# Optimization experiments

Hardware: AMD Instinct MI355X
Metric: run time of the kernel (lower is better)

## Reference

```python
import jax, jax.numpy as jnp
import numpy as np

NUM_USERS = 100000
NUM_ITEMS = 50000
EMB_DIM = 64
NNZ = 4800000
BATCH = 16384
N_LAYERS = 3


def setup_inputs() -> dict:
    key = jax.random.key(0)
    k0, k1, k2, k3, k4, k5 = jax.random.split(key, 6)
    N = NUM_USERS + NUM_ITEMS
    rows = jax.random.randint(k0, (NNZ,), 0, N, dtype=jnp.int32)
    cols = jax.random.randint(k1, (NNZ,), 0, N, dtype=jnp.int32)
    # symmetric normalization values: 1/sqrt(deg_out * deg_in), as in LightGCN preprocessing
    ones = jnp.ones((NNZ,), jnp.float32)
    deg_r = jax.ops.segment_sum(ones, rows, num_segments=N)
    deg_c = jax.ops.segment_sum(ones, cols, num_segments=N)
    vals = 1.0 / jnp.sqrt(jnp.maximum(deg_r[rows], 1.0) * jnp.maximum(deg_c[cols], 1.0))
    user_emb = 0.1 * jax.random.normal(k2, (NUM_USERS, EMB_DIM), jnp.float32)
    item_emb = 0.1 * jax.random.normal(k3, (NUM_ITEMS, EMB_DIM), jnp.float32)
    user_idx = jax.random.randint(k4, (BATCH,), 0, NUM_USERS, dtype=jnp.int64)
    item_idx = jax.random.randint(k5, (BATCH,), 0, NUM_ITEMS, dtype=jnp.int64)
    return {
        "user_emb": user_emb,
        "item_emb": item_emb,
        "rows": rows,
        "cols": cols,
        "vals": vals,
        "user_idx": user_idx,
        "item_idx": item_idx,
        "n_layers": N_LAYERS,
    }


def reference(user_emb, item_emb, rows, cols, vals, user_idx, item_idx, n_layers):
    num_users = user_emb.shape[0]
    N = num_users + item_emb.shape[0]
    all_emb = jnp.concatenate([user_emb, item_emb], axis=0)  # [N, D]
    acc = all_emb  # running sum over layer embeddings (embs[0] = E)
    emb = all_emb
    for _ in range(n_layers):
        # SpMM: out[r] = sum_{edges (r,c)} vals * emb[c]
        emb = jax.ops.segment_sum(vals[:, None] * emb[cols], rows, num_segments=N)
        acc = acc + emb
    light_out = acc / jnp.float32(n_layers + 1)  # mean over stacked layers
    u_e = light_out[user_idx]                     # [B, D]
    i_e = light_out[num_users + item_idx]         # [B, D]
    return (u_e * i_e).sum(axis=-1)               # [B]
```

## Files before the change

### kernel.cpp

```cpp
#include <hip/hip_runtime.h>
#include <hip/hip_fp16.h>

#define NUM_USERS 100000
#define NUM_ITEMS 50000
#define NN (NUM_USERS + NUM_ITEMS)
#define EMB_DIM 64
#define BATCH 16384
#define RPA 512
#define NBA ((NN + RPA - 1) / RPA)
#define SLOT 22528
#define NBLKA 768
#define CAP 16
#define OVF 32
#define SENT (1 << 27)
#define RSLOT 72
#define RPB 256
#define LSLOT 64
#define NBB (NBA * 2)

__device__ __forceinline__ unsigned h2u(__half2 h) {
    union { __half2 h; unsigned u; } x; x.h = h; return x.u;
}
__device__ __forceinline__ __half2 u2h(unsigned u) {
    union { __half2 h; unsigned u; } x; x.u = u; return x.h;
}

__global__ void lgcn_prep(unsigned long long* __restrict__ gq,
                          unsigned char* __restrict__ flags) {
    int i = blockIdx.x * blockDim.x + threadIdx.x;
    if (i < NBA) gq[i] = 0;
    for (int j = i; j < NN / 4; j += gridDim.x * blockDim.x)
        ((unsigned*)flags)[j] = 0;
    if (i == 0)
        for (int j = (NN / 4) * 4; j < NN; ++j) flags[j] = 0;
}

__global__ void __launch_bounds__(512) lgcn_binA(
        const float4* __restrict__ user_emb, const float4* __restrict__ item_emb,
        uint2* __restrict__ embh, int n_user4, int n_tot4,
        const int* __restrict__ rows, const int* __restrict__ cols,
        const float* __restrict__ vals, unsigned long long* __restrict__ gq,
        int2* __restrict__ cv_tmp, int nnz, int epb) {
    __shared__ int2 stage[CAP][NBA];
    __shared__ int  hist[NBA];
    __shared__ int  SBase[NBA];
    __shared__ int  pcnt[NBA];
    __shared__ int4 ovfBuf[2][OVF];
    __shared__ int  ovfCnt[2];
    int t = threadIdx.x;

    for (int i = blockIdx.x * 512 + t; i < n_tot4; i += NBLKA * 512) {
        float4 v = (i < n_user4) ? user_emb[i] : item_emb[i - n_user4];
        uint2 o;
        o.x = h2u(__float22half2_rn(make_float2(v.x, v.y)));
        o.y = h2u(__float22half2_rn(make_float2(v.z, v.w)));
        embh[i] = o;
    }

    int base = blockIdx.x * epb;
    int end  = base + epb; if (end > nnz) end = nnz;
    if (t < NBA) { hist[t] = 0; pcnt[t] = 0; }
    if (t == 0) { ovfCnt[0] = 0; ovfCnt[1] = 0; }
    __syncthreads();
    for (int i = base + t; i < end; i += 512)
        atomicAdd(&hist[rows[i] >> 9], 1);
    __syncthreads();
    if (t < NBA) {
        int c = hist[t];
        int p = 0;
        if (c) {
            int cp = (c + 7) & ~7;
            unsigned long long old = atomicAdd(&gq[t],
                ((unsigned long long)c << 32) | (unsigned)cp);
            p = (int)(unsigned)old;
        }
        SBase[t] = p;
    }
    __syncthreads();

    int p = 0;
    for (int r0 = base; r0 < end; r0 += 1024, p ^= 1) {
        int no = ovfCnt[p ^ 1];
        for (int j = t; j < no; j += 512) {
            int4 e = ovfBuf[p ^ 1][j];
            int b = e.w;
            int k = atomicAdd(&pcnt[b], 1);
            if (k < CAP) stage[k][b] = make_int2(e.x, e.y);
            else { int q = atomicAdd(&ovfCnt[p], 1);
                   if (q < OVF) ovfBuf[p][q] = e; }
        }
#pragma unroll
        for (int q2 = 0; q2 < 2; ++q2) {
            int i = r0 + q2 * 512 + t;
            if (i < end) {
                int r = rows[i];
                int b = r >> 9;
                __half hv = __float2half(vals[i]);
                int ex = ((r & 511) << 18) | cols[i];
                int ey = (int)h2u(__half2half2(hv));
                int k = atomicAdd(&pcnt[b], 1);
                if (k < CAP) stage[k][b] = make_int2(ex, ey);
                else { int q = atomicAdd(&ovfCnt[p], 1);
                       if (q < OVF) ovfBuf[p][q] = make_int4(ex, ey, 0, b); }
            }
        }
        __syncthreads();
        if (t < NBA) {
            int c = pcnt[t]; if (c > CAP) c = CAP;
            int g = c & ~7;
            if (g) {
                long long gb = (long long)t * SLOT + SBase[t];
                int4* dst = (int4*)&cv_tmp[gb];
                for (int j = 0; j < g; j += 2) {
                    int2 e0 = stage[j][t];
                    int2 e1 = stage[j + 1][t];
                    dst[j >> 1] = make_int4(e0.x, e0.y, e1.x, e1.y);
                }
                SBase[t] += g;
                for (int j = g; j < c; ++j) stage[j - g][t] = stage[j][t];
            }
            pcnt[t] = c - g;
        }
        if (t == 0) ovfCnt[p ^ 1] = 0;
        __syncthreads();
    }

    {
        int no = ovfCnt[p ^ 1];
        for (int j = t; j < no; j += 512) {
            int4 e = ovfBuf[p ^ 1][j];
            int b = e.w;
            int k = atomicAdd(&pcnt[b], 1);
            if (k < CAP) stage[k][b] = make_int2(e.x, e.y);
            else cv_tmp[(long long)b * SLOT + SBase[b] + k] =
                     make_int2(e.x, e.y);
        }
    }
    __syncthreads();
    if (t < NBA) {
        int c_raw = pcnt[t];
        int cl = min(c_raw, CAP);
        long long gb = (long long)t * SLOT + SBase[t];
        for (int j = 0; j < cl; ++j) cv_tmp[gb + j] = stage[j][t];
        int cp = (c_raw + 7) & ~7;
        for (int j = c_raw; j < cp; ++j) cv_tmp[gb + j] = make_int2(SENT, 0);
    }
}

#define BPUT(p) do { int x = (p).x; if (!(x & SENT)) {                       \
    int rl9 = (x >> 18) & 511;                                               \
    if ((rl9 & 256) == hsel) { int rl = rl9 & 255;                           \
        int pos = atomicAdd(&cnt[rl], 1);                                    \
        int v16 = (p).y & 0xFFFF;                                            \
        int pk = (((v16 + 2) >> 2) << 18) | (x & 0x3FFFF);                   \
        if (pos < LSLOT) slot[rl][pos] = pk;                                 \
        else if (pos < RSLOT)                                                \
            cv[(long long)(r0 + rl) * RSLOT + pos] = pk; } } } while (0)

__global__ void __launch_bounds__(1024) lgcn_binB(
        const unsigned long long* __restrict__ gq,
        const int2* __restrict__ cv_tmp, int* __restrict__ cv,
        int* __restrict__ deg,
        const int* __restrict__ user_idx, const int* __restrict__ item_idx,
        unsigned char* __restrict__ flags) {
    __shared__ int slot[RPB][LSLOT];
    __shared__ int cnt[RPB];
    int s    = blockIdx.x >> 1;
    int half = blockIdx.x & 1;
    int t = threadIdx.x;
    long long w0 = (long long)s * SLOT;
    int wlen = (int)(unsigned)gq[s];
    int r0 = s * RPA + half * RPB;
    int hsel = half << 8;
    for (int j = t; j < RPB; j += 1024) cnt[j] = 0;
    __syncthreads();
    int i = t;
    for (; i + 3 * 1024 < wlen; i += 4096) {
        int2 p0 = cv_tmp[w0 + i];
        int2 p1 = cv_tmp[w0 + i + 1024];
        int2 p2 = cv_tmp[w0 + i + 2048];
        int2 p3 = cv_tmp[w0 + i + 3072];
        BPUT(p0); BPUT(p1); BPUT(p2); BPUT(p3);
    }
    for (; i < wlen; i += 1024) {
        int2 p = cv_tmp[w0 + i];
        BPUT(p);
    }
    for (int j = blockIdx.x * 1024 + t; j < BATCH; j += NBB * 1024) {
        flags[user_idx[j]] = 1;
        flags[NUM_USERS + item_idx[j]] = 1;
    }
    __syncthreads();
    for (int j = t; j < RPB; j += 1024) deg[r0 + j] = min(cnt[j], RSLOT);
    for (int g = t; g < RPB * (LSLOT / 4); g += 1024) {
        int rl = g >> 4, q = g & 15;
        int4 v = *(int4*)&slot[rl][q * 4];
        *(int4*)&cv[(long long)(r0 + rl) * RSLOT + q * 4] = v;
    }
}

__device__ __forceinline__ unsigned eidx(int p, int dim8) {
    return ((unsigned)p & 0x3FFFFu) * 8u + (unsigned)dim8;
}
__device__ __forceinline__ void efma(int p, uint4 raw,
        __half2& c0, __half2& c1, __half2& c2, __half2& c3) {
    unsigned vv = ((unsigned)p >> 18) << 2;
    __half2 v2 = u2h(vv | (vv << 16));
    c0 = __hfma2(v2, u2h(raw.x), c0);
    c1 = __hfma2(v2, u2h(raw.y), c1);
    c2 = __hfma2(v2, u2h(raw.z), c2);
    c3 = __hfma2(v2, u2h(raw.w), c3);
}

__global__ void __launch_bounds__(256) lgcn_spmm(
        const int* __restrict__ deg,
        const int* __restrict__ cv,
        const uint4* __restrict__ embh,
        uint4* __restrict__ nxth,
        const unsigned char* __restrict__ flags, int sel,
        const uint4* __restrict__ e0t, const uint4* __restrict__ e1t,
        float4* __restrict__ sums) {
    int wid = (blockIdx.x * blockDim.x + threadIdx.x) >> 6;
    int lane = threadIdx.x & 63;
    if (wid >= NN) return;
    if (sel && !flags[wid]) return;
    int n = deg[wid];
    int grp  = lane >> 3;
    int dim8 = lane & 7;
    const int* ep = cv + wid * RSLOT;

    __half2 c0 = __float2half2_rn(0.f);
    __half2 c1 = c0, c2 = c0, c3 = c0;

    int nb = n >> 5;
    if (nb == 2) {
        int4 pa = *(const int4*)&ep[4 * grp];
        int4 pb = *(const int4*)&ep[32 + 4 * grp];
        uint4 ra0 = embh[eidx(pa.x, dim8)];
        uint4 ra1 = embh[eidx(pa.y, dim8)];
        uint4 ra2 = embh[eidx(pa.z, dim8)];
        uint4 ra3 = embh[eidx(pa.w, dim8)];
        uint4 rb0 = embh[eidx(pb.x, dim8)];
        uint4 rb1 = embh[eidx(pb.y, dim8)];
        uint4 rb2 = embh[eidx(pb.z, dim8)];
        uint4 rb3 = embh[eidx(pb.w, dim8)];
        efma(pa.x, ra0, c0, c1, c2, c3);
        efma(pa.y, ra1, c0, c1, c2, c3);
        efma(pa.z, ra2, c0, c1, c2, c3);
        efma(pa.w, ra3, c0, c1, c2, c3);
        efma(pb.x, rb0, c0, c1, c2, c3);
        efma(pb.y, rb1, c0, c1, c2, c3);
        efma(pb.z, rb2, c0, c1, c2, c3);
        efma(pb.w, rb3, c0, c1, c2, c3);
    } else if (nb == 1) {
        int4 pa = *(const int4*)&ep[4 * grp];
        uint4 ra0 = embh[eidx(pa.x, dim8)];
        uint4 ra1 = embh[eidx(pa.y, dim8)];
        uint4 ra2 = embh[eidx(pa.z, dim8)];
        uint4 ra3 = embh[eidx(pa.w, dim8)];
        efma(pa.x, ra0, c0, c1, c2, c3);
        efma(pa.y, ra1, c0, c1, c2, c3);
        efma(pa.z, ra2, c0, c1, c2, c3);
        efma(pa.w, ra3, c0, c1, c2, c3);
    }
    const int* et = ep + (nb << 5);
    int rem = n & 31;
    if (rem & 16) {
        int2 p2 = *(const int2*)&et[2 * grp];
        uint4 ra = embh[eidx(p2.x, dim8)];
        uint4 rb = embh[eidx(p2.y, dim8)];
        efma(p2.x, ra, c0, c1, c2, c3);
        efma(p2.y, rb, c0, c1, c2, c3);
        et += 16;
    }
    if (rem & 8) {
        int pp = et[grp];
        uint4 rr = embh[eidx(pp, dim8)];
        efma(pp, rr, c0, c1, c2, c3);
        et += 8;
    }
    int r7 = rem & 7;
    if (grp < r7) {
        int pp = et[grp];
        uint4 rr = embh[eidx(pp, dim8)];
        efma(pp, rr, c0, c1, c2, c3);
    }

#pragma unroll
    for (int off = 8; off < 64; off <<= 1) {
        c0 = __hadd2(c0, u2h(__shfl_xor(h2u(c0), off)));
        c1 = __hadd2(c1, u2h(__shfl_xor(h2u(c1), off)));
        c2 = __hadd2(c2, u2h(__shfl_xor(h2u(c2), off)));
        c3 = __hadd2(c3, u2h(__shfl_xor(h2u(c3), off)));
    }
    if (grp == 0) {
        int o = wid * 8 + dim8;
        if (!sel) {
            uint4 ov;
            ov.x = h2u(c0); ov.y = h2u(c1); ov.z = h2u(c2); ov.w = h2u(c3);
            nxth[o] = ov;
        } else {
            uint4 r0v = e0t[o], r1v = e1t[o], r2v = embh[o];
            float2 f0 = __half22float2(c0), f1 = __half22float2(c1);
            float2 f2 = __half22float2(c2), f3 = __half22float2(c3);
            float2 a;
            a = __half22float2(u2h(r0v.x)); f0.x += a.x; f0.y += a.y;
            a = __half22float2(u2h(r1v.x)); f0.x += a.x; f0.y += a.y;
            a = __half22float2(u2h(r2v.x)); f0.x += a.x; f0.y += a.y;
            a = __half22float2(u2h(r0v.y)); f1.x += a.x; f1.y += a.y;
            a = __half22float2(u2h(r1v.y)); f1.x += a.x; f1.y += a.y;
            a = __half22float2(u2h(r2v.y)); f1.x += a.x; f1.y += a.y;
            a = __half22float2(u2h(r0v.z)); f2.x += a.x; f2.y += a.y;
            a = __half22float2(u2h(r1v.z)); f2.x += a.x; f2.y += a.y;
            a = __half22float2(u2h(r2v.z)); f2.x += a.x; f2.y += a.y;
            a = __half22float2(u2h(r0v.w)); f3.x += a.x; f3.y += a.y;
            a = __half22float2(u2h(r1v.w)); f3.x += a.x; f3.y += a.y;
            a = __half22float2(u2h(r2v.w)); f3.x += a.x; f3.y += a.y;
            int so = wid * 16 + dim8 * 2;
            sums[so]     = make_float4(f0.x, f0.y, f1.x, f1.y);
            sums[so + 1] = make_float4(f2.x, f2.y, f3.x, f3.y);
        }
    }
}

__global__ void lgcn_dot(const float4* __restrict__ sums,
                         const int* __restrict__ user_idx,
                         const int* __restrict__ item_idx,
                         float* __restrict__ out, int batch) {
    int t = blockIdx.x * blockDim.x + threadIdx.x;
    int b = t >> 4;
    if (b >= batch) return;
    int l = t & 15;
    float4 su = sums[(long long)user_idx[b] * 16 + l];
    float4 si = sums[(long long)(NUM_USERS + item_idx[b]) * 16 + l];
    float s = su.x * si.x + su.y * si.y + su.z * si.z + su.w * si.w;
    s += __shfl_down(s, 8, 16);
    s += __shfl_down(s, 4, 16);
    s += __shfl_down(s, 2, 16);
    s += __shfl_down(s, 1, 16);
    if (l == 0) out[b] = s * (1.0f / 16.0f);
}

extern "C" void kernel_launch(void* const* d_in, const int* in_sizes, int n_in,
                              void* d_out, int out_size, void* d_ws, size_t ws_size,
                              hipStream_t stream) {
    const float* user_emb = (const float*)d_in[0];
    const float* item_emb = (const float*)d_in[1];
    const int*   rows     = (const int*)d_in[2];
    const int*   cols     = (const int*)d_in[3];
    const float* vals     = (const float*)d_in[4];
    const int*   user_idx = (const int*)d_in[5];
    const int*   item_idx = (const int*)d_in[6];
    float* out = (float*)d_out;

    const int nnz = in_sizes[2];
    const size_t node_uint2 = (size_t)NN * 16;

    uint2* E[4];
    E[0] = (uint2*)d_ws;
    E[1] = E[0] + node_uint2;
    E[2] = E[1] + node_uint2;
    E[3] = E[2] + node_uint2;
    int*    cv   = (int*)(E[3] + node_uint2);
    float4* sums = (float4*)(cv + (size_t)NN * RSLOT);
    int*    deg  = (int*)(sums + (size_t)NN * 16);
    unsigned long long* gq = (unsigned long long*)(deg + NN);
    unsigned char* flags = (unsigned char*)(gq + NBA);
    int2*   cv_tmp = (int2*)E[1];

    const int n_tot4  = NN * EMB_DIM / 4;
    const int n_user4 = NUM_USERS * EMB_DIM / 4;
    const int epb = (nnz + NBLKA - 1) / NBLKA;

    lgcn_prep<<<64, 256, 0, stream>>>(gq, flags);

    lgcn_binA<<<NBLKA, 512, 0, stream>>>(
        (const float4*)user_emb, (const float4*)item_emb, E[0],
        n_user4, n_tot4, rows, cols, vals, gq, cv_tmp, nnz, epb);

    lgcn_binB<<<NBB, 1024, 0, stream>>>(gq, cv_tmp, cv, deg,
                                        user_idx, item_idx, flags);

    const int spmm_blocks = (NN * 64 + 255) / 256;
    for (int layer = 0; layer < 3; ++layer) {
        lgcn_spmm<<<spmm_blocks, 256, 0, stream>>>(deg, cv,
                                                   (const uint4*)E[layer],
                                                   (uint4*)E[layer + 1],
                                                   flags, layer == 2 ? 1 : 0,
                                                   (const uint4*)E[0],
                                                   (const uint4*)E[1], sums);
    }

    lgcn_dot<<<(BATCH * 16 + 255) / 256, 256, 0, stream>>>(
        sums, user_idx, item_idx, out, BATCH);
}
```

Baseline: 390.9 us.

## Fuse first SpMM into binning kernel and last layer into batch dot

Layer-1 SpMM now runs inside the binB kernel, reading each row's edge list straight from shared memory right after binning, which removes one full SpMM launch and a pass over the cv array. The final layer is computed only for batch rows inside a new dot kernel that also sums the layer embeddings, which removes the flags array, its clearing, the sums buffer and the separate dot kernel. The catch is that binB runs a serial per-warp row loop without unrolled gathers. Batch rows are also recomputed whenever an index repeats.

```diff
diff --git a/kernel.cpp b/kernel.cpp
--- a/kernel.cpp
+++ b/kernel.cpp
@@ -24,15 +24,22 @@
 __device__ __forceinline__ __half2 u2h(unsigned u) {
     union { __half2 h; unsigned u; } x; x.u = u; return x.h;
 }
-
-__global__ void lgcn_prep(unsigned long long* __restrict__ gq,
-                          unsigned char* __restrict__ flags) {
+__device__ __forceinline__ unsigned eidx(int p, int dim8) {
+    return ((unsigned)p & 0x3FFFFu) * 8u + (unsigned)dim8;
+}
+__device__ __forceinline__ void efma(int p, uint4 raw,
+        __half2& c0, __half2& c1, __half2& c2, __half2& c3) {
+    unsigned vv = ((unsigned)p >> 18) << 2;
+    __half2 v2 = u2h(vv | (vv << 16));
+    c0 = __hfma2(v2, u2h(raw.x), c0);
+    c1 = __hfma2(v2, u2h(raw.y), c1);
+    c2 = __hfma2(v2, u2h(raw.z), c2);
+    c3 = __hfma2(v2, u2h(raw.w), c3);
+}
+
+__global__ void lgcn_prep(unsigned long long* __restrict__ gq) {
     int i = blockIdx.x * blockDim.x + threadIdx.x;
     if (i < NBA) gq[i] = 0;
-    for (int j = i; j < NN / 4; j += gridDim.x * blockDim.x)
-        ((unsigned*)flags)[j] = 0;
-    if (i == 0)
-        for (int j = (NN / 4) * 4; j < NN; ++j) flags[j] = 0;
 }
 
 __global__ void __launch_bounds__(512) lgcn_binA(
@@ -155,14 +162,14 @@
         int pk = (((v16 + 2) >> 2) << 18) | (x & 0x3FFFF);                   \
         if (pos < LSLOT) slot[rl][pos] = pk;                                 \
         else if (pos < RSLOT)                                                \
-            cv[(long long)(r0 + rl) * RSLOT + pos] = pk; } } } while (0)
-
-__global__ void __launch_bounds__(1024) lgcn_binB(
+            cv[(r0 + rl) * RSLOT + pos] = pk; } } } while (0)
+
+__global__ void __launch_bounds__(1024) lgcn_binBspmm1(
         const unsigned long long* __restrict__ gq,
         const int2* __restrict__ cv_tmp, int* __restrict__ cv,
         int* __restrict__ deg,
-        const int* __restrict__ user_idx, const int* __restrict__ item_idx,
-        unsigned char* __restrict__ flags) {
+        const uint4* __restrict__ embh,
+        uint4* __restrict__ outB) {
     __shared__ int slot[RPB][LSLOT];
     __shared__ int cnt[RPB];
     int s    = blockIdx.x >> 1;
@@ -186,44 +193,60 @@
         int2 p = cv_tmp[w0 + i];
         BPUT(p);
     }
-    for (int j = blockIdx.x * 1024 + t; j < BATCH; j += NBB * 1024) {
-        flags[user_idx[j]] = 1;
-        flags[NUM_USERS + item_idx[j]] = 1;
-    }
-    __syncthreads();
-    for (int j = t; j < RPB; j += 1024) deg[r0 + j] = min(cnt[j], RSLOT);
+    __syncthreads();
+    for (int j = t; j < RPB; j += 1024)
+        if (r0 + j < NN) deg[r0 + j] = min(cnt[j], RSLOT);
     for (int g = t; g < RPB * (LSLOT / 4); g += 1024) {
         int rl = g >> 4, q = g & 15;
-        int4 v = *(int4*)&slot[rl][q * 4];
-        *(int4*)&cv[(long long)(r0 + rl) * RSLOT + q * 4] = v;
-    }
-}
-
-__device__ __forceinline__ unsigned eidx(int p, int dim8) {
-    return ((unsigned)p & 0x3FFFFu) * 8u + (unsigned)dim8;
-}
-__device__ __forceinline__ void efma(int p, uint4 raw,
-        __half2& c0, __half2& c1, __half2& c2, __half2& c3) {
-    unsigned vv = ((unsigned)p >> 18) << 2;
-    __half2 v2 = u2h(vv | (vv << 16));
-    c0 = __hfma2(v2, u2h(raw.x), c0);
-    c1 = __hfma2(v2, u2h(raw.y), c1);
-    c2 = __hfma2(v2, u2h(raw.z), c2);
-    c3 = __hfma2(v2, u2h(raw.w), c3);
+        if (r0 + rl < NN) {
+            int4 v = *(int4*)&slot[rl][q * 4];
+            *(int4*)&cv[(r0 + rl) * RSLOT + q * 4] = v;
+        }
+    }
+    int w = t >> 6, lane = t & 63;
+    int grp = lane >> 3, dim8 = lane & 7;
+    for (int rr = w * 16; rr < w * 16 + 16; ++rr) {
+        int r = r0 + rr;
+        if (r >= NN) continue;
+        int n = min(cnt[rr], RSLOT);
+        __half2 c0 = __float2half2_rn(0.f);
+        __half2 c1 = c0, c2 = c0, c3 = c0;
+        int m = n >> 3;
+        for (int k = 0; k < m; ++k) {
+            int j = 8 * k + grp;
+            int p = (j < LSLOT) ? slot[rr][j] : cv[r * RSLOT + j];
+            uint4 raw = embh[eidx(p, dim8)];
+            efma(p, raw, c0, c1, c2, c3);
+        }
+        if (grp < (n & 7)) {
+            int j = 8 * m + grp;
+            int p = (j < LSLOT) ? slot[rr][j] : cv[r * RSLOT + j];
+            uint4 raw = embh[eidx(p, dim8)];
+            efma(p, raw, c0, c1, c2, c3);
+        }
+#pragma unroll
+        for (int off = 8; off < 64; off <<= 1) {
+            c0 = __hadd2(c0, u2h(__shfl_xor(h2u(c0), off)));
+            c1 = __hadd2(c1, u2h(__shfl_xor(h2u(c1), off)));
+            c2 = __hadd2(c2, u2h(__shfl_xor(h2u(c2), off)));
+            c3 = __hadd2(c3, u2h(__shfl_xor(h2u(c3), off)));
+        }
+        if (grp == 0) {
+            uint4 ov;
+            ov.x = h2u(c0); ov.y = h2u(c1); ov.z = h2u(c2); ov.w = h2u(c3);
+            outB[r * 8 + dim8] = ov;
+        }
+    }
 }
 
 __global__ void __launch_bounds__(256) lgcn_spmm(
         const int* __restrict__ deg,
         const int* __restrict__ cv,
         const uint4* __restrict__ embh,
-        uint4* __restrict__ nxth,
-        const unsigned char* __restrict__ flags, int sel,
-        const uint4* __restrict__ e0t, const uint4* __restrict__ e1t,
-        float4* __restrict__ sums) {
+        uint4* __restrict__ nxth) {
     int wid = (blockIdx.x * blockDim.x + threadIdx.x) >> 6;
     int lane = threadIdx.x & 63;
     if (wid >= NN) return;
-    if (sel && !flags[wid]) return;
     int n = deg[wid];
     int grp  = lane >> 3;
     int dim8 = lane & 7;
@@ -294,51 +317,79 @@
         c3 = __hadd2(c3, u2h(__shfl_xor(h2u(c3), off)));
     }
     if (grp == 0) {
-        int o = wid * 8 + dim8;
-        if (!sel) {
-            uint4 ov;
-            ov.x = h2u(c0); ov.y = h2u(c1); ov.z = h2u(c2); ov.w = h2u(c3);
-            nxth[o] = ov;
-        } else {
-            uint4 r0v = e0t[o], r1v = e1t[o], r2v = embh[o];
-            float2 f0 = __half22float2(c0), f1 = __half22float2(c1);
-            float2 f2 = __half22float2(c2), f3 = __half22float2(c3);
-            float2 a;
-            a = __half22float2(u2h(r0v.x)); f0.x += a.x; f0.y += a.y;
-            a = __half22float2(u2h(r1v.x)); f0.x += a.x; f0.y += a.y;
-            a = __half22float2(u2h(r2v.x)); f0.x += a.x; f0.y += a.y;
-            a = __half22float2(u2h(r0v.y)); f1.x += a.x; f1.y += a.y;
-            a = __half22float2(u2h(r1v.y)); f1.x += a.x; f1.y += a.y;
-            a = __half22float2(u2h(r2v.y)); f1.x += a.x; f1.y += a.y;
-            a = __half22float2(u2h(r0v.z)); f2.x += a.x; f2.y += a.y;
-            a = __half22float2(u2h(r1v.z)); f2.x += a.x; f2.y += a.y;
-            a = __half22float2(u2h(r2v.z)); f2.x += a.x; f2.y += a.y;
-            a = __half22float2(u2h(r0v.w)); f3.x += a.x; f3.y += a.y;
-            a = __half22float2(u2h(r1v.w)); f3.x += a.x; f3.y += a.y;
-            a = __half22float2(u2h(r2v.w)); f3.x += a.x; f3.y += a.y;
-            int so = wid * 16 + dim8 * 2;
-            sums[so]     = make_float4(f0.x, f0.y, f1.x, f1.y);
-            sums[so + 1] = make_float4(f2.x, f2.y, f3.x, f3.y);
-        }
-    }
-}
-
-__global__ void lgcn_dot(const float4* __restrict__ sums,
-                         const int* __restrict__ user_idx,
-                         const int* __restrict__ item_idx,
-                         float* __restrict__ out, int batch) {
-    int t = blockIdx.x * blockDim.x + threadIdx.x;
-    int b = t >> 4;
-    if (b >= batch) return;
-    int l = t & 15;
-    float4 su = sums[(long long)user_idx[b] * 16 + l];
-    float4 si = sums[(long long)(NUM_USERS + item_idx[b]) * 16 + l];
-    float s = su.x * si.x + su.y * si.y + su.z * si.z + su.w * si.w;
-    s += __shfl_down(s, 8, 16);
-    s += __shfl_down(s, 4, 16);
-    s += __shfl_down(s, 2, 16);
-    s += __shfl_down(s, 1, 16);
-    if (l == 0) out[b] = s * (1.0f / 16.0f);
+        uint4 ov;
+        ov.x = h2u(c0); ov.y = h2u(c1); ov.z = h2u(c2); ov.w = h2u(c3);
+        nxth[wid * 8 + dim8] = ov;
+    }
+}
+
+__device__ __forceinline__ void d3row(const int* __restrict__ cv,
+        const int* __restrict__ deg, const uint4* __restrict__ C,
+        const uint4* __restrict__ A, const uint4* __restrict__ B,
+        int r, int grp, int dim8,
+        float2& f0, float2& f1, float2& f2, float2& f3) {
+    int n = deg[r];
+    const int* ep = cv + r * RSLOT;
+    __half2 c0 = __float2half2_rn(0.f);
+    __half2 c1 = c0, c2 = c0, c3 = c0;
+    int m = n >> 3;
+    for (int k = 0; k < m; ++k) {
+        int p = ep[8 * k + grp];
+        uint4 raw = C[eidx(p, dim8)];
+        efma(p, raw, c0, c1, c2, c3);
+    }
+    if (grp < (n & 7)) {
+        int p = ep[8 * m + grp];
+        uint4 raw = C[eidx(p, dim8)];
+        efma(p, raw, c0, c1, c2, c3);
+    }
+#pragma unroll
+    for (int off = 8; off < 64; off <<= 1) {
+        c0 = __hadd2(c0, u2h(__shfl_xor(h2u(c0), off)));
+        c1 = __hadd2(c1, u2h(__shfl_xor(h2u(c1), off)));
+        c2 = __hadd2(c2, u2h(__shfl_xor(h2u(c2), off)));
+        c3 = __hadd2(c3, u2h(__shfl_xor(h2u(c3), off)));
+    }
+    f0 = __half22float2(c0); f1 = __half22float2(c1);
+    f2 = __half22float2(c2); f3 = __half22float2(c3);
+    int o = r * 8 + dim8;
+    uint4 ra = A[o], rb = B[o], rc = C[o];
+    float2 a;
+    a = __half22float2(u2h(ra.x)); f0.x += a.x; f0.y += a.y;
+    a = __half22float2(u2h(rb.x)); f0.x += a.x; f0.y += a.y;
+    a = __half22float2(u2h(rc.x)); f0.x += a.x; f0.y += a.y;
+    a = __half22float2(u2h(ra.y)); f1.x += a.x; f1.y += a.y;
+    a = __half22float2(u2h(rb.y)); f1.x += a.x; f1.y += a.y;
+    a = __half22float2(u2h(rc.y)); f1.x += a.x; f1.y += a.y;
+    a = __half22float2(u2h(ra.z)); f2.x += a.x; f2.y += a.y;
+    a = __half22float2(u2h(rb.z)); f2.x += a.x; f2.y += a.y;
+    a = __half22float2(u2h(rc.z)); f2.x += a.x; f2.y += a.y;
+    a = __half22float2(u2h(ra.w)); f3.x += a.x; f3.y += a.y;
+    a = __half22float2(u2h(rb.w)); f3.x += a.x; f3.y += a.y;
+    a = __half22float2(u2h(rc.w)); f3.x += a.x; f3.y += a.y;
+}
+
+__global__ void __launch_bounds__(256) lgcn_dot3(
+        const int* __restrict__ deg, const int* __restrict__ cv,
+        const uint4* __restrict__ C, const uint4* __restrict__ A,
+        const uint4* __restrict__ B,
+        const int* __restrict__ user_idx, const int* __restrict__ item_idx,
+        float* __restrict__ out) {
+    int wid = (blockIdx.x * blockDim.x + threadIdx.x) >> 6;
+    int lane = threadIdx.x & 63;
+    if (wid >= BATCH) return;
+    int grp = lane >> 3, dim8 = lane & 7;
+    int u  = user_idx[wid];
+    int it = NUM_USERS + item_idx[wid];
+    float2 u0, u1, u2, u3, i0, i1, i2, i3;
+    d3row(cv, deg, C, A, B, u,  grp, dim8, u0, u1, u2, u3);
+    d3row(cv, deg, C, A, B, it, grp, dim8, i0, i1, i2, i3);
+    float s = u0.x * i0.x + u0.y * i0.y + u1.x * i1.x + u1.y * i1.y
+            + u2.x * i2.x + u2.y * i2.y + u3.x * i3.x + u3.y * i3.y;
+    s += __shfl_xor(s, 1);
+    s += __shfl_xor(s, 2);
+    s += __shfl_xor(s, 4);
+    if (lane == 0) out[wid] = s * (1.0f / 16.0f);
 }
 
 extern "C" void kernel_launch(void* const* d_in, const int* in_sizes, int n_in,
@@ -356,41 +407,32 @@
     const int nnz = in_sizes[2];
     const size_t node_uint2 = (size_t)NN * 16;
 
-    uint2* E[4];
-    E[0] = (uint2*)d_ws;
-    E[1] = E[0] + node_uint2;
-    E[2] = E[1] + node_uint2;
-    E[3] = E[2] + node_uint2;
-    int*    cv   = (int*)(E[3] + node_uint2);
-    float4* sums = (float4*)(cv + (size_t)NN * RSLOT);
-    int*    deg  = (int*)(sums + (size_t)NN * 16);
+    uint2* A    = (uint2*)d_ws;
+    uint2* Cslt = A + node_uint2;
+    int2*  cv_tmp = (int2*)Cslt;
+    int*   cv   = (int*)(A + 4 * node_uint2);
+    uint2* B    = (uint2*)(cv + (size_t)NN * RSLOT);
+    int*   deg  = (int*)(B + node_uint2);
     unsigned long long* gq = (unsigned long long*)(deg + NN);
-    unsigned char* flags = (unsigned char*)(gq + NBA);
-    int2*   cv_tmp = (int2*)E[1];
 
     const int n_tot4  = NN * EMB_DIM / 4;
     const int n_user4 = NUM_USERS * EMB_DIM / 4;
     const int epb = (nnz + NBLKA - 1) / NBLKA;
 
-    lgcn_prep<<<64, 256, 0, stream>>>(gq, flags);
+    lgcn_prep<<<2, 256, 0, stream>>>(gq);
 
     lgcn_binA<<<NBLKA, 512, 0, stream>>>(
-        (const float4*)user_emb, (const float4*)item_emb, E[0],
+        (const float4*)user_emb, (const float4*)item_emb, A,
         n_user4, n_tot4, rows, cols, vals, gq, cv_tmp, nnz, epb);
 
-    lgcn_binB<<<NBB, 1024, 0, stream>>>(gq, cv_tmp, cv, deg,
-                                        user_idx, item_idx, flags);
+    lgcn_binBspmm1<<<NBB, 1024, 0, stream>>>(gq, cv_tmp, cv, deg,
+                                             (const uint4*)A, (uint4*)B);
 
     const int spmm_blocks = (NN * 64 + 255) / 256;
-    for (int layer = 0; layer < 3; ++layer) {
-        lgcn_spmm<<<spmm_blocks, 256, 0, stream>>>(deg, cv,
-                                                   (const uint4*)E[layer],
-                                                   (uint4*)E[layer + 1],
-                                                   flags, layer == 2 ? 1 : 0,
-                                                   (const uint4*)E[0],
-                                                   (const uint4*)E[1], sums);
-    }
-
-    lgcn_dot<<<(BATCH * 16 + 255) / 256, 256, 0, stream>>>(
-        sums, user_idx, item_idx, out, BATCH);
-}
+    lgcn_spmm<<<spmm_blocks, 256, 0, stream>>>(deg, cv,
+                                               (const uint4*)B, (uint4*)Cslt);
+
+    lgcn_dot3<<<(BATCH * 64 + 255) / 256, 256, 0, stream>>>(
+        deg, cv, (const uint4*)Cslt, (const uint4*)A, (const uint4*)B,
+        user_idx, item_idx, out);
+}
```

Result: no change. 385.7 us (-1.3%).
